# Performance work log

Measured on AMD Instinct MI355X. Metric: run time of the kernel, lower is better.

The kernel has to match this reference:

```python
import jax, jax.numpy as jnp
import numpy as np

IMG = 256          # RasterizationSettings.image_size
CHUNK = 64         # faces per scan step (bounds peak memory)
B_N, V_N, F_N = 1, 5023, 9976   # FLAME head mesh: 5023 verts / 9976 faces
BIG = 1e10
EPS = 1e-8
AMB, DIF, SPC = 0.5, 0.3, 0.2   # PointLights default ambient/diffuse/specular
SHININESS = 64.0                # Materials default shininess
LIGHT = (0.0, 0.0, 3.0)         # PointLights(location=[[0,0,3]])


def setup_inputs() -> dict:
    key = jax.random.key(0)
    kv, kf = jax.random.split(key)
    vertices = 0.15 * jax.random.normal(kv, (B_N, V_N, 3), jnp.float32)
    R = jnp.tile(jnp.eye(3, dtype=jnp.float32)[None], (B_N, 1, 1))
    T = jnp.tile(jnp.array([0.0, 0.0, 1.2], jnp.float32)[None], (B_N, 1))
    tm = jnp.zeros((B_N, 4, 4), jnp.float32)
    tm = tm.at[:, :3, :3].set(R).at[:, :3, 3].set(T).at[:, 3, 3].set(1.0)
    focal_length = jnp.full((B_N, 2), 1.5 * IMG, jnp.float32)  # screen-space focal
    faces = jax.random.randint(kf, (F_N, 3), 0, V_N, dtype=jnp.int32)
    return {"vertices": vertices, "transform_matrix": tm,
            "focal_length": focal_length, "faces": faces}


def _normalize(x):
    return x / (jnp.linalg.norm(x, axis=-1, keepdims=True) + EPS)


def _render(vertices, transform_matrix, focal_length, faces):
    B, V, _ = vertices.shape
    H = W = IMG
    HW = H * W
    R = transform_matrix[:, :3, :3]
    T = transform_matrix[:, :3, 3]

    # world -> view (PyTorch3D row-vector convention), then pinhole NDC projection
    v_view = jnp.einsum('bvi,bij->bvj', vertices, R) + T[:, None, :]
    z = v_view[..., 2]                                   # [B,V] view-space depth
    zc = jnp.maximum(z, EPS)
    fx = (2.0 * focal_length[:, 0] / W)[:, None]         # screen -> NDC focal
    fy = (2.0 * focal_length[:, 1] / H)[:, None]
    x_ndc = fx * v_view[..., 0] / zc
    y_ndc = fy * v_view[..., 1] / zc

    # pixel grid in NDC (PyTorch3D: +X left, +Y up)
    xs = 1.0 - 2.0 * (jnp.arange(W, dtype=jnp.float32) + 0.5) / W
    ys = 1.0 - 2.0 * (jnp.arange(H, dtype=jnp.float32) + 0.5) / H
    px = jnp.broadcast_to(xs[None, :], (H, W)).reshape(HW)
    py = jnp.broadcast_to(ys[:, None], (H, W)).reshape(HW)

    # pad faces to a multiple of CHUNK; gather per-face vertex coords
    F = faces.shape[0]
    nC = -(-F // CHUNK)
    Fp = nC * CHUNK
    fpad = jnp.concatenate([faces, jnp.zeros((Fp - F, 3), faces.dtype)], axis=0)
    fvalid = (jnp.arange(Fp) < F).reshape(nC, CHUNK)
    tri_x = x_ndc[:, fpad].reshape(B, nC, CHUNK, 3).transpose(1, 0, 2, 3)
    tri_y = y_ndc[:, fpad].reshape(B, nC, CHUNK, 3).transpose(1, 0, 2, 3)
    tri_z = z[:, fpad].reshape(B, nC, CHUNK, 3).transpose(1, 0, 2, 3)
    fidx = jnp.arange(Fp, dtype=jnp.int32).reshape(nC, CHUNK)

    # hard z-buffer rasterization (faces_per_pixel=1, blur_radius=0) via scan
    def step(carry, inp):
        zbuf, bestf, bb0, bb1 = carry
        tx, ty, tz, valid, fid = inp                    # tx/ty/tz: [B,CHUNK,3]
        x0, x1, x2 = (tx[..., i][:, None, :] for i in range(3))   # [B,1,C]
        y0, y1, y2 = (ty[..., i][:, None, :] for i in range(3))
        area = (x1 - x0) * (y2 - y0) - (x2 - x0) * (y1 - y0)
        P, Q = px[None, :, None], py[None, :, None]     # [1,HW,1]
        w0 = (x1 - P) * (y2 - Q) - (x2 - P) * (y1 - Q)  # [B,HW,C] edge fns
        w1 = (x2 - P) * (y0 - Q) - (x0 - P) * (y2 - Q)
        w2 = area - w0 - w1
        denom = jnp.where(jnp.abs(area) > EPS, area, 1.0)
        b0, b1, b2 = w0 / denom, w1 / denom, w2 / denom
        z0, z1, z2 = (jnp.maximum(tz[..., i], EPS)[:, None, :] for i in range(3))
        zok = (tz > EPS).all(-1)[:, None, :]
        inside = ((b0 >= 0) & (b1 >= 0) & (b2 >= 0)
                  & (jnp.abs(area) > EPS) & zok & valid[None, None, :])
        t0, t1 = b0 / z0, b1 / z1
        invz = t0 + t1 + b2 / z2
        zpix = 1.0 / jnp.maximum(invz, EPS)             # perspective-correct depth
        depth = jnp.where(inside, zpix, BIG)
        j = jnp.argmin(depth, axis=2)                   # nearest face in chunk [B,HW]
        d = jnp.take_along_axis(depth, j[..., None], 2)[..., 0]
        p0 = jnp.take_along_axis(t0 * zpix, j[..., None], 2)[..., 0]
        p1 = jnp.take_along_axis(t1 * zpix, j[..., None], 2)[..., 0]
        fh = fid[j]
        keep = d < zbuf
        return (jnp.where(keep, d, zbuf), jnp.where(keep, fh, bestf),
                jnp.where(keep, p0, bb0), jnp.where(keep, p1, bb1)), None

    init = (jnp.full((B, HW), BIG, jnp.float32), jnp.zeros((B, HW), jnp.int32),
            jnp.zeros((B, HW), jnp.float32), jnp.zeros((B, HW), jnp.float32))
    (zbuf, bestf, b0, b1), _ = jax.lax.scan(step, init, (tri_x, tri_y, tri_z, fvalid, fidx))
    hit = zbuf < (0.5 * BIG)
    bary = jnp.stack([b0, b1, 1.0 - b0 - b1], axis=-1)  # [B,HW,3] persp-correct

    # vertex normals (area-weighted face-normal scatter)
    fverts = vertices[:, faces]                         # [B,F,3,3]
    fnorm = jnp.cross(fverts[:, :, 1] - fverts[:, :, 0],
                      fverts[:, :, 2] - fverts[:, :, 0])
    vn = jnp.zeros_like(vertices)
    for i in range(3):
        vn = vn.at[:, faces[:, i]].add(fnorm)
    vn = _normalize(vn)

    # per-pixel interpolation + SoftPhongShader math (white vertex texture)
    pf = fpad[bestf]                                    # [B,HW,3] vertex ids
    gather = jax.vmap(lambda tbl, idx: tbl[idx])        # ([V,3],[HW,3])->[HW,3,3]
    pv = gather(vertices, pf)
    pn = gather(vn, pf)
    Pw = jnp.einsum('bpk,bpkc->bpc', bary, pv)          # world position
    Nw = _normalize(jnp.einsum('bpk,bpkc->bpc', bary, pn))
    cam = -jnp.einsum('bj,bkj->bk', T, R)               # camera center (R orthonormal)
    Ld = _normalize(jnp.array(LIGHT, jnp.float32)[None, None] - Pw)
    Vd = _normalize(cam[:, None] - Pw)
    ndl = jnp.maximum(jnp.sum(Nw * Ld, -1), 0.0)
    refl = -Ld + 2.0 * jnp.sum(Nw * Ld, -1, keepdims=True) * Nw
    spec = jnp.maximum(jnp.sum(refl * Vd, -1), 0.0) ** SHININESS
    shade = AMB + DIF * ndl + SPC * spec                # equal across RGB channels
    rgb = jnp.broadcast_to(shade[..., None], (B, HW, 3))
    alpha = hit.astype(jnp.float32)
    rgb = jnp.where(hit[..., None], rgb, 1.0)           # white background
    rgb = jnp.where(alpha[..., None] < 0.5, 0.0, rgb) * 255.0  # images[alpha<0.5]=0; *255
    images = rgb.reshape(B, H, W, 3).transpose(0, 3, 1, 2)
    return images, alpha.reshape(B, 1, H, W)


def reference(vertices, transform_matrix, focal_length, faces):
    return _render(vertices, transform_matrix, focal_length, faces)
```

## Files before the change

### kernel.cpp

```cpp
#include <hip/hip_runtime.h>
#include <math.h>

#define IMGSZ 256
#define HW (IMGSZ * IMGSZ)
#define EPSF 1e-8f
#define BIGF 1e10f
#define SLICE_LEN 1024
#define MARG 1e-4f
#define CAP 8192
#define SEGLEN 128
#define RBLOCKS 2048
#define SENTINEL 0x501502F9FFFFFFFFull

__global__ void k_transform(const float* __restrict__ verts,
                            const float* __restrict__ tm,
                            const float* __restrict__ focal,
                            float* __restrict__ xn, float* __restrict__ yn,
                            float* __restrict__ zv, float* __restrict__ vnacc,
                            unsigned long long* __restrict__ zb,
                            int* __restrict__ cnt, int V) {
#pragma clang fp contract(off)
    int i = blockIdx.x * blockDim.x + threadIdx.x;
    int nth = gridDim.x * blockDim.x;
    for (int j = i; j < HW; j += nth) zb[j] = SENTINEL;
    if (i < 256) cnt[i] = 0;
    if (i >= V) return;
    float vx = verts[i * 3 + 0], vy = verts[i * 3 + 1], vz = verts[i * 3 + 2];
    float xv = ((vx * tm[0] + vy * tm[4]) + vz * tm[8]) + tm[3];
    float yv = ((vx * tm[1] + vy * tm[5]) + vz * tm[9]) + tm[7];
    float zw = ((vx * tm[2] + vy * tm[6]) + vz * tm[10]) + tm[11];
    float zc = fmaxf(zw, EPSF);
    float fx = 2.0f * focal[0] / (float)IMGSZ;
    float fy = 2.0f * focal[1] / (float)IMGSZ;
    xn[i] = fx * xv / zc;
    yn[i] = fy * yv / zc;
    zv[i] = zw;
    vnacc[i * 3 + 0] = 0.0f;
    vnacc[i * 3 + 1] = 0.0f;
    vnacc[i * 3 + 2] = 0.0f;
}

__global__ void k_facesetup(const int* __restrict__ faces,
                            const float* __restrict__ verts,
                            const float* __restrict__ xn,
                            const float* __restrict__ yn,
                            const float* __restrict__ zv,
                            float4* __restrict__ fd,
                            float* __restrict__ vnacc, int F) {
#pragma clang fp contract(off)
    int f = blockIdx.x * blockDim.x + threadIdx.x;
    if (f >= F) return;
    int i0 = faces[f * 3 + 0], i1 = faces[f * 3 + 1], i2 = faces[f * 3 + 2];
    float x0 = xn[i0], x1 = xn[i1], x2 = xn[i2];
    float y0 = yn[i0], y1 = yn[i1], y2 = yn[i2];
    float z0 = zv[i0], z1 = zv[i1], z2 = zv[i2];
    float area = (x1 - x0) * (y2 - y0) - (x2 - x0) * (y1 - y0);
    bool zok = (z0 > EPSF) && (z1 > EPSF) && (z2 > EPSF);
    float areaStore = zok ? area : 0.0f;
    float z0c = fmaxf(z0, EPSF), z1c = fmaxf(z1, EPSF), z2c = fmaxf(z2, EPSF);
    float zminb = fminf(fminf(z0c, z1c), z2c) * (1.0f - 1e-5f);
    fd[f * 3 + 0] = make_float4(x0, y0, x1, y1);
    fd[f * 3 + 1] = make_float4(x2, y2, areaStore, __int_as_float(f));
    fd[f * 3 + 2] = make_float4(z0c, z1c, z2c, zminb);
    float a0 = verts[i0 * 3 + 0], a1 = verts[i0 * 3 + 1], a2 = verts[i0 * 3 + 2];
    float b0 = verts[i1 * 3 + 0], b1 = verts[i1 * 3 + 1], b2 = verts[i1 * 3 + 2];
    float c0 = verts[i2 * 3 + 0], c1 = verts[i2 * 3 + 1], c2 = verts[i2 * 3 + 2];
    float e1x = b0 - a0, e1y = b1 - a1, e1z = b2 - a2;
    float e2x = c0 - a0, e2y = c1 - a1, e2z = c2 - a2;
    float nx = e1y * e2z - e1z * e2y;
    float ny = e1z * e2x - e1x * e2z;
    float nz = e1x * e2y - e1y * e2x;
    atomicAdd(&vnacc[i0 * 3 + 0], nx);
    atomicAdd(&vnacc[i0 * 3 + 1], ny);
    atomicAdd(&vnacc[i0 * 3 + 2], nz);
    atomicAdd(&vnacc[i1 * 3 + 0], nx);
    atomicAdd(&vnacc[i1 * 3 + 1], ny);
    atomicAdd(&vnacc[i1 * 3 + 2], nz);
    atomicAdd(&vnacc[i2 * 3 + 0], nx);
    atomicAdd(&vnacc[i2 * 3 + 1], ny);
    atomicAdd(&vnacc[i2 * 3 + 2], nz);
}

__device__ __forceinline__ void tile_bounds(int tileX, int tileY,
                                            float& txmin, float& txmax,
                                            float& tymin, float& tymax) {
#pragma clang fp contract(off)
    txmax = 1.0f - 2.0f * ((float)(tileX * 16) + 0.5f) / (float)IMGSZ;
    txmin = 1.0f - 2.0f * ((float)(tileX * 16 + 15) + 0.5f) / (float)IMGSZ;
    tymax = 1.0f - 2.0f * ((float)(tileY * 16) + 0.5f) / (float)IMGSZ;
    tymin = 1.0f - 2.0f * ((float)(tileY * 16 + 15) + 0.5f) / (float)IMGSZ;
}

__device__ __forceinline__ int zbucket(float zminb) {
    float v = (zminb - 0.4f) * 40.0f;
    int b = (int)v;
    if (v < 0.0f) b = 0;
    if (b > 63) b = 63;
    return b;
}
__device__ __forceinline__ float bucketlo(float zminb) {
    int b = zbucket(zminb);
    return (b == 0) ? 0.0f : (0.4f + 0.025f * (float)b - 1e-4f);
}

__device__ __forceinline__ bool rect_cull(float x0, float y0, float x1, float y1,
                                          float x2, float y2, float area,
                                          float rxmin, float rxmax,
                                          float rymin, float rymax) {
#pragma clang fp contract(off)
    const float M = 1e-4f;
    float mnx = fminf(fminf(x0, x1), x2);
    float mxx = fmaxf(fmaxf(x0, x1), x2);
    float mny = fminf(fminf(y0, y1), y2);
    float mxy = fmaxf(fmaxf(y0, y1), y2);
    bool pass = (mnx <= rxmax + M) && (mxx >= rxmin - M) &&
                (mny <= rymax + M) && (mxy >= rymin - M);
    if (!pass) return false;
    float a0 = y1 - y2, bb0 = x2 - x1, k0 = x1 * y2 - x2 * y1;
    float a1 = y2 - y0, bb1 = x0 - x2, k1 = x2 * y0 - x0 * y2;
    float a2 = y0 - y1, bb2 = x1 - x0, k2 = x0 * y1 - x1 * y0;
    if (area > 0.0f) {
        float w0m = k0 + fmaxf(a0 * rxmin, a0 * rxmax) + fmaxf(bb0 * rymin, bb0 * rymax);
        float w1m = k1 + fmaxf(a1 * rxmin, a1 * rxmax) + fmaxf(bb1 * rymin, bb1 * rymax);
        float w2m = k2 + fmaxf(a2 * rxmin, a2 * rxmax) + fmaxf(bb2 * rymin, bb2 * rymax);
        return (w0m >= -MARG) && (w1m >= -MARG) && (w2m >= -MARG);
    } else {
        float w0m = k0 + fminf(a0 * rxmin, a0 * rxmax) + fminf(bb0 * rymin, bb0 * rymax);
        float w1m = k1 + fminf(a1 * rxmin, a1 * rxmax) + fminf(bb1 * rymin, bb1 * rymax);
        float w2m = k2 + fminf(a2 * rxmin, a2 * rxmax) + fminf(bb2 * rymin, bb2 * rymax);
        return (w0m <= MARG) && (w1m <= MARG) && (w2m <= MARG);
    }
}

__launch_bounds__(256)
__global__ void k_bincull(const float4* __restrict__ fd, int F,
                          int* __restrict__ cnt, int* __restrict__ bins,
                          unsigned long long* __restrict__ zb) {
#pragma clang fp contract(off)
    __shared__ int scnt[4];
    __shared__ int sbase;
    int t = threadIdx.x;
    int lane = t & 63, wid = t >> 6;
    int tile = blockIdx.x >> 2;
    int q = blockIdx.x & 3;
    int tileX = tile & 15, tileY = tile >> 4;
    float txmin, txmax, tymin, tymax;
    tile_bounds(tileX, tileY, txmin, txmax, tymin, tymax);
    int Fq = (F + 3) >> 2;
    int fbeg = q * Fq;
    int fend = min(F, fbeg + Fq);
    int binbase = tile * CAP;

    for (int base = fbeg; base < fend; base += 256) {
        int f = base + t;
        bool pass = false;
        float x0, y0, x1, y1, x2, y2, area;
        float4 Bv;
        if (f < fend) {
            float4 A = fd[f * 3 + 0];
            Bv = fd[f * 3 + 1];
            area = Bv.z;
            if (fabsf(area) > EPSF) {
                x0 = A.x; y0 = A.y; x1 = A.z; y1 = A.w; x2 = Bv.x; y2 = Bv.y;
                pass = rect_cull(x0, y0, x1, y1, x2, y2, area,
                                 txmin, txmax, tymin, tymax);
            }
        }
        unsigned long long m = __ballot(pass);
        if (lane == 0) scnt[wid] = __popcll(m);
        __syncthreads();
        int off = 0;
#pragma unroll
        for (int w = 0; w < 4; ++w)
            if (w < wid) off += scnt[w];
        int total = scnt[0] + scnt[1] + scnt[2] + scnt[3];
        if (t == 0) sbase = (total > 0) ? atomicAdd(&cnt[tile], total) : 0;
        __syncthreads();
        int sb = sbase;
        if (pass) {
            int rank = __popcll(m & ((1ull << lane) - 1ull));
            int s = sb + off + rank;
            if (s < CAP) {
                bins[binbase + s] = f;
            } else {
                float4 c = fd[f * 3 + 2];
                for (int p = 0; p < 256; ++p) {
                    int colp = tileX * 16 + (p & 15), rowp = tileY * 16 + (p >> 4);
                    float P = 1.0f - 2.0f * ((float)colp + 0.5f) / (float)IMGSZ;
                    float Q = 1.0f - 2.0f * ((float)rowp + 0.5f) / (float)IMGSZ;
                    float e0x = x0 - P, e0y = y0 - Q;
                    float e1x = x1 - P, e1y = y1 - Q;
                    float e2x = x2 - P, e2y = y2 - Q;
                    float w0 = e1x * e2y - e2x * e1y;
                    float w1 = e2x * e0y - e0x * e2y;
                    float w2 = (area - w0) - w1;
                    bool inside = (area > 0.0f) ? (w0 >= 0.0f && w1 >= 0.0f && w2 >= 0.0f)
                                                : (w0 <= 0.0f && w1 <= 0.0f && w2 <= 0.0f);
                    if (inside) {
                        float b0v = w0 / area, b1v = w1 / area, b2v = w2 / area;
                        float t0 = b0v / c.x, t1 = b1v / c.y, t2v = b2v / c.z;
                        float invz = (t0 + t1) + t2v;
                        float zpix = 1.0f / fmaxf(invz, EPSF);
                        unsigned long long pk =
                            ((unsigned long long)(unsigned int)__float_as_int(zpix) << 32) |
                            (unsigned int)__float_as_int(Bv.w);
                        atomicMin(&zb[rowp * IMGSZ + colp], pk);
                    }
                }
            }
        }
        __syncthreads();
    }
}

__launch_bounds__(256)
__global__ void k_binsort(const float* __restrict__ fdf,
                          const int* __restrict__ cnt,
                          int* __restrict__ bins,
                          unsigned short* __restrict__ workl,
                          int* __restrict__ worktotal) {
    __shared__ int sfid[CAP];
    __shared__ unsigned char sbkt[CAP];
    __shared__ int hist[64], hbase[64];
    __shared__ int sn[256], snseg[256], sord[256], spre[256];
    int t = threadIdx.x;
    if (blockIdx.x == 256) {
        int n = cnt[t];
        if (n > CAP) n = CAP;
        int ns = (n > 0) ? (n + SEGLEN - 1) / SEGLEN : 0;
        sn[t] = n;
        snseg[t] = ns;
        __syncthreads();
        int r = 0;
        for (int k = 0; k < 256; ++k) {
            int nk = sn[k];
            r += (nk > n) || (nk == n && k < t);
        }
        sord[r] = t;
        __syncthreads();
        if (t == 0) {
            int run = 0;
            for (int k = 0; k < 256; ++k) { spre[k] = run; run += snseg[sord[k]]; }
            *worktotal = run;
        }
        __syncthreads();
        int tile = sord[t];
        int base = spre[t];
        int ns2 = snseg[tile];
        for (int seg = 0; seg < ns2; ++seg)
            workl[base + seg] = (unsigned short)((tile << 6) | seg);
        return;
    }
    int tile = blockIdx.x;
    int n = cnt[tile];
    if (n > CAP) n = CAP;
    if (n == 0) return;
    int nseg = (n + SEGLEN - 1) / SEGLEN;
    if (t < 64) hist[t] = 0;
    __syncthreads();
    for (int i = t; i < n; i += 256) {
        int f = bins[tile * CAP + i];
        sfid[i] = f;
        float zminb = fdf[f * 12 + 11];
        int b = zbucket(zminb);
        sbkt[i] = (unsigned char)b;
        atomicAdd(&hist[b], 1);
    }
    __syncthreads();
    if (t == 0) {
        int run = 0;
        for (int k = 0; k < 64; ++k) { hbase[k] = run; run += hist[k]; }
    }
    __syncthreads();
    if (t < 64) hist[t] = 0;
    __syncthreads();
    for (int i = t; i < n; i += 256) {
        int b = sbkt[i];
        int pos = hbase[b] + atomicAdd(&hist[b], 1);
        int tpos = (pos % nseg) * SEGLEN + pos / nseg;
        bins[tile * CAP + tpos] = sfid[i];
    }
}

__launch_bounds__(256)
__global__ void k_rastseg(const float4* __restrict__ fd,
                          const int* __restrict__ cnt,
                          const int* __restrict__ bins,
                          const unsigned short* __restrict__ workl,
                          const int* __restrict__ worktotal,
                          unsigned long long* __restrict__ zb) {
#pragma clang fp contract(off)
    __shared__ float4 sA[64], sB[64], sC[64];
    __shared__ int sdone[4];
    int total = *worktotal;
    int wave = threadIdx.x >> 6;
    int lane = threadIdx.x & 63;
    int t = threadIdx.x;
    for (int wi = blockIdx.x; wi < total; wi += gridDim.x) {
        int w = workl[wi];
        int tile = w >> 6, seg = w & 63;
        int n = cnt[tile];
        if (n > CAP) n = CAP;
        int nseg = (n + SEGLEN - 1) / SEGLEN;
        int nb = (n - 1 - seg) / nseg + 1;
        int binbase = tile * CAP + seg * SEGLEN;

        int tileX = tile & 15, tileY = tile >> 4;
        int col0 = tileX * 16 + ((wave & 1) << 3);
        int row0 = tileY * 16 + ((wave >> 1) << 3);
        int col = col0 + (lane & 7);
        int row = row0 + (lane >> 3);
        int pix = row * IMGSZ + col;
        float P = 1.0f - 2.0f * ((float)col + 0.5f) / (float)IMGSZ;
        float Q = 1.0f - 2.0f * ((float)row + 0.5f) / (float)IMGSZ;
        float sxmax = 1.0f - 2.0f * ((float)col0 + 0.5f) / (float)IMGSZ;
        float sxmin = 1.0f - 2.0f * ((float)(col0 + 7) + 0.5f) / (float)IMGSZ;
        float symax = 1.0f - 2.0f * ((float)row0 + 0.5f) / (float)IMGSZ;
        float symin = 1.0f - 2.0f * ((float)(row0 + 7) + 0.5f) / (float)IMGSZ;

        unsigned long long seed = zb[pix];
        unsigned long long bestpk = seed;
        float bestz = __uint_as_float((unsigned int)(seed >> 32));
        bool done = false;
        if (lane == 0) sdone[wave] = 0;

        for (int k0 = 0; k0 < nb; k0 += 64) {
            int cnum = min(64, nb - k0);
            __syncthreads();
            if (sdone[0] + sdone[1] + sdone[2] + sdone[3] == 4) break;
            if (t < 192) {
                int part = t >> 6, fi = t & 63;
                if (fi < cnum) {
                    int f = bins[binbase + k0 + fi];
                    float4 v = fd[f * 3 + part];
                    if (part == 0) sA[fi] = v;
                    else if (part == 1) sB[fi] = v;
                    else sC[fi] = v;
                }
            }
            __syncthreads();
            if (!done) {
                bool pass8 = false;
                if (lane < cnum) {
                    float4 ra = sA[lane], rb = sB[lane];
                    float area = rb.z;
                    if (fabsf(area) > EPSF)
                        pass8 = rect_cull(ra.x, ra.y, ra.z, ra.w, rb.x, rb.y,
                                          area, sxmin, sxmax, symin, symax);
                }
                unsigned long long mm = __ballot(pass8);
                int it = 0;
                while (mm) {
                    int s = __ffsll(mm) - 1;
                    mm &= mm - 1;
                    float4 cc = sC[s];
                    if ((it++ & 7) == 0) {
                        if (__all(bucketlo(cc.w) > bestz)) {
                            done = true;
                            if (lane == 0) sdone[wave] = 1;
                            break;
                        }
                    }
                    float4 a = sA[s], b = sB[s];
                    float area = b.z;
                    float e0x = a.x - P, e0y = a.y - Q;
                    float e1x = a.z - P, e1y = a.w - Q;
                    float e2x = b.x - P, e2y = b.y - Q;
                    float w0 = e1x * e2y - e2x * e1y;
                    float w1 = e2x * e0y - e0x * e2y;
                    float w2 = (area - w0) - w1;
                    bool inside = (area > 0.0f) ? (w0 >= 0.0f && w1 >= 0.0f && w2 >= 0.0f)
                                                : (w0 <= 0.0f && w1 <= 0.0f && w2 <= 0.0f);
                    bool want = inside && !(cc.w > bestz);
                    if (want) {
                        float b0v = w0 / area, b1v = w1 / area, b2v = w2 / area;
                        float t0 = b0v / cc.x, t1 = b1v / cc.y, t2v = b2v / cc.z;
                        float invz = (t0 + t1) + t2v;
                        float zpix = 1.0f / fmaxf(invz, EPSF);
                        unsigned long long pk =
                            ((unsigned long long)(unsigned int)__float_as_int(zpix) << 32) |
                            (unsigned int)__float_as_int(b.w);
                        if (pk < bestpk) {
                            bestpk = pk;
                            bestz = zpix;
                        }
                    }
                }
            }
        }
        if (bestpk < seed) atomicMin(&zb[pix], bestpk);
        __syncthreads();
    }
}

__launch_bounds__(256)
__global__ void k_raster_mono(const float4* __restrict__ fd, int F,
                              unsigned long long* __restrict__ zb) {
#pragma clang fp contract(off)
    __shared__ float4 sfd[256 * 3];
    __shared__ int scnt[4];
    int t = threadIdx.x;
    int lane = t & 63, wid = t >> 6;
    int tile = blockIdx.x & 255;
    int slice = blockIdx.x >> 8;
    int tileX = tile & 15, tileY = tile >> 4;
    int col = tileX * 16 + (t & 15);
    int row = tileY * 16 + (t >> 4);
    int pix = row * IMGSZ + col;
    float P = 1.0f - 2.0f * ((float)col + 0.5f) / (float)IMGSZ;
    float Q = 1.0f - 2.0f * ((float)row + 0.5f) / (float)IMGSZ;
    float txmin, txmax, tymin, tymax;
    tile_bounds(tileX, tileY, txmin, txmax, tymin, tymax);
    int fbeg = slice * SLICE_LEN;
    int fend = fbeg + SLICE_LEN;
    if (fend > F) fend = F;
    unsigned long long bestpk = SENTINEL;
    float bestz = BIGF;
    for (int base = fbeg; base < fend; base += 256) {
        unsigned long long ext = zb[pix];
        if (ext < bestpk) {
            bestpk = ext;
            bestz = __uint_as_float((unsigned int)(ext >> 32));
        }
        int f = base + t;
        bool pass = false;
        float4 A, B, C;
        if (f < fend) {
            A = fd[f * 3 + 0];
            B = fd[f * 3 + 1];
            C = fd[f * 3 + 2];
            float area = B.z;
            if (fabsf(area) > EPSF)
                pass = rect_cull(A.x, A.y, A.z, A.w, B.x, B.y, area,
                                 txmin, txmax, tymin, tymax);
        }
        unsigned long long m = __ballot(pass);
        if (lane == 0) scnt[wid] = __popcll(m);
        __syncthreads();
        int off = 0;
#pragma unroll
        for (int w = 0; w < 4; ++w)
            if (w < wid) off += scnt[w];
        int total = scnt[0] + scnt[1] + scnt[2] + scnt[3];
        if (pass) {
            int rank = __popcll(m & ((1ull << lane) - 1ull));
            int s = off + rank;
            sfd[s * 3 + 0] = A;
            sfd[s * 3 + 1] = B;
            sfd[s * 3 + 2] = C;
        }
        __syncthreads();
        for (int s = 0; s < total; ++s) {
            float4 a = sfd[s * 3 + 0], b = sfd[s * 3 + 1], c = sfd[s * 3 + 2];
            float e0x = a.x - P, e0y = a.y - Q;
            float e1x = a.z - P, e1y = a.w - Q;
            float e2x = b.x - P, e2y = b.y - Q;
            float w0 = e1x * e2y - e2x * e1y;
            float w1 = e2x * e0y - e0x * e2y;
            float area = b.z;
            float w2 = (area - w0) - w1;
            bool inside = (area > 0.0f) ? (w0 >= 0.0f && w1 >= 0.0f && w2 >= 0.0f)
                                        : (w0 <= 0.0f && w1 <= 0.0f && w2 <= 0.0f);
            bool want = inside && !(c.w > bestz);
            if (want) {
                float b0v = w0 / area, b1v = w1 / area, b2v = w2 / area;
                float t0 = b0v / c.x, t1 = b1v / c.y, t2v = b2v / c.z;
                float invz = (t0 + t1) + t2v;
                float zpix = 1.0f / fmaxf(invz, EPSF);
                unsigned long long pk =
                    ((unsigned long long)(unsigned int)__float_as_int(zpix) << 32) |
                    (unsigned int)__float_as_int(b.w);
                if (pk < bestpk) {
                    bestpk = pk;
                    bestz = zpix;
                }
            }
        }
        if (bestpk < ext) atomicMin(&zb[pix], bestpk);
        __syncthreads();
    }
}

__launch_bounds__(256)
__global__ void k_shade(const unsigned long long* __restrict__ zb,
                        const float4* __restrict__ fd,
                        const int* __restrict__ faces,
                        const float* __restrict__ verts,
                        const float* __restrict__ vn,
                        const float* __restrict__ tm,
                        float* __restrict__ out) {
#pragma clang fp contract(off)
    int pix = blockIdx.x * 256 + threadIdx.x;
    unsigned long long pk = zb[pix];
    float depth = __uint_as_float((unsigned int)(pk >> 32));
    float val = 0.0f, alpha = 0.0f;
    if (depth < 0.5f * BIGF) {
        int bestf = (int)(unsigned int)(pk & 0xFFFFFFFFull);
        int col = pix & (IMGSZ - 1), row = pix >> 8;
        float P = 1.0f - 2.0f * ((float)col + 0.5f) / (float)IMGSZ;
        float Q = 1.0f - 2.0f * ((float)row + 0.5f) / (float)IMGSZ;
        float4 a = fd[bestf * 3 + 0], b = fd[bestf * 3 + 1], c = fd[bestf * 3 + 2];
        float e0x = a.x - P, e0y = a.y - Q;
        float e1x = a.z - P, e1y = a.w - Q;
        float e2x = b.x - P, e2y = b.y - Q;
        float w0 = e1x * e2y - e2x * e1y;
        float w1 = e2x * e0y - e0x * e2y;
        float area = b.z;
        float t0 = (w0 / area) / c.x, t1 = (w1 / area) / c.y;
        float t2v = (((area - w0) - w1) / area) / c.z;
        float invz = (t0 + t1) + t2v;
        float zpix = 1.0f / fmaxf(invz, EPSF);
        float bp0 = t0 * zpix, bp1 = t1 * zpix;

        int i0 = faces[bestf * 3 + 0], i1 = faces[bestf * 3 + 1], i2 = faces[bestf * 3 + 2];
        float b0v = bp0, b1v = bp1, b2v = (1.0f - bp0) - bp1;
        float Pwx = (b0v * verts[i0 * 3 + 0] + b1v * verts[i1 * 3 + 0]) + b2v * verts[i2 * 3 + 0];
        float Pwy = (b0v * verts[i0 * 3 + 1] + b1v * verts[i1 * 3 + 1]) + b2v * verts[i2 * 3 + 1];
        float Pwz = (b0v * verts[i0 * 3 + 2] + b1v * verts[i1 * 3 + 2]) + b2v * verts[i2 * 3 + 2];
        float v0x = vn[i0 * 3 + 0], v0y = vn[i0 * 3 + 1], v0z = vn[i0 * 3 + 2];
        float n0 = sqrtf((v0x * v0x + v0y * v0y) + v0z * v0z) + EPSF;
        v0x /= n0; v0y /= n0; v0z /= n0;
        float v1x = vn[i1 * 3 + 0], v1y = vn[i1 * 3 + 1], v1z = vn[i1 * 3 + 2];
        float n1 = sqrtf((v1x * v1x + v1y * v1y) + v1z * v1z) + EPSF;
        v1x /= n1; v1y /= n1; v1z /= n1;
        float v2x = vn[i2 * 3 + 0], v2y = vn[i2 * 3 + 1], v2z = vn[i2 * 3 + 2];
        float n2 = sqrtf((v2x * v2x + v2y * v2y) + v2z * v2z) + EPSF;
        v2x /= n2; v2y /= n2; v2z /= n2;
        float Nx = (b0v * v0x + b1v * v1x) + b2v * v2x;
        float Ny = (b0v * v0y + b1v * v1y) + b2v * v2y;
        float Nz = (b0v * v0z + b1v * v1z) + b2v * v2z;
        float nn = sqrtf((Nx * Nx + Ny * Ny) + Nz * Nz) + EPSF;
        Nx /= nn; Ny /= nn; Nz /= nn;
        float T0 = tm[3], T1 = tm[7], T2 = tm[11];
        float camx = -((T0 * tm[0] + T1 * tm[1]) + T2 * tm[2]);
        float camy = -((T0 * tm[4] + T1 * tm[5]) + T2 * tm[6]);
        float camz = -((T0 * tm[8] + T1 * tm[9]) + T2 * tm[10]);
        float Ldx = 0.0f - Pwx, Ldy = 0.0f - Pwy, Ldz = 3.0f - Pwz;
        float ln = sqrtf((Ldx * Ldx + Ldy * Ldy) + Ldz * Ldz) + EPSF;
        Ldx /= ln; Ldy /= ln; Ldz /= ln;
        float Vx = camx - Pwx, Vy = camy - Pwy, Vz = camz - Pwz;
        float vv = sqrtf((Vx * Vx + Vy * Vy) + Vz * Vz) + EPSF;
        Vx /= vv; Vy /= vv; Vz /= vv;
        float dt = (Nx * Ldx + Ny * Ldy) + Nz * Ldz;
        float ndl = fmaxf(dt, 0.0f);
        float twodt = 2.0f * dt;
        float rx = -Ldx + twodt * Nx;
        float ry = -Ldy + twodt * Ny;
        float rz = -Ldz + twodt * Nz;
        float sdot = (rx * Vx + ry * Vy) + rz * Vz;
        float sb = fmaxf(sdot, 0.0f);
        float s2 = sb * sb, s4 = s2 * s2, s8 = s4 * s4, s16 = s8 * s8, s32 = s16 * s16;
        float spec = s32 * s32;
        float shade = (0.5f + 0.3f * ndl) + 0.2f * spec;
        val = shade * 255.0f;
        alpha = 1.0f;
    }
    out[0 * HW + pix] = val;
    out[1 * HW + pix] = val;
    out[2 * HW + pix] = val;
    out[3 * HW + pix] = alpha;
}

extern "C" void kernel_launch(void* const* d_in, const int* in_sizes, int n_in,
                              void* d_out, int out_size, void* d_ws, size_t ws_size,
                              hipStream_t stream) {
    const float* verts = (const float*)d_in[0];
    const float* tm = (const float*)d_in[1];
    const float* focal = (const float*)d_in[2];
    const int* faces = (const int*)d_in[3];
    int V = in_sizes[0] / 3;
    int F = in_sizes[3] / 3;

    char* base = (char*)d_ws;
    unsigned long long* zb = (unsigned long long*)base;
    int* cnt = (int*)(base + (size_t)HW * 8);
    float* xn = (float*)(base + (size_t)HW * 8 + 4096);
    float* yn = xn + V;
    float* zv = xn + 2 * (size_t)V;
    float* vn = xn + 3 * (size_t)V;
    size_t fdByte = ((size_t)HW * 8 + 4096 + 6 * (size_t)V * 4 + 15) & ~(size_t)15;
    float4* fd = (float4*)(base + fdByte);
    size_t binByte = fdByte + (size_t)F * 48;
    int* bins = (int*)(base + binByte);
    size_t workByte = binByte + (size_t)256 * CAP * 4;
    unsigned short* workl = (unsigned short*)(base + workByte);
    int* worktotal = (int*)(base + workByte + 16384 * 2);
    size_t needBinned = workByte + 16384 * 2 + 64;
    float* out = (float*)d_out;

    int vb = (V + 255) / 256;
    int fb = (F + 255) / 256;
    k_transform<<<vb, 256, 0, stream>>>(verts, tm, focal, xn, yn, zv, vn, zb, cnt, V);
    k_facesetup<<<fb, 256, 0, stream>>>(faces, verts, xn, yn, zv, fd, vn, F);
    if (ws_size >= needBinned) {
        k_bincull<<<256 * 4, 256, 0, stream>>>(fd, F, cnt, bins, zb);
        k_binsort<<<257, 256, 0, stream>>>((const float*)fd, cnt, bins, workl, worktotal);
        k_rastseg<<<RBLOCKS, 256, 0, stream>>>(fd, cnt, bins, workl, worktotal, zb);
    } else {
        int nslice = (F + SLICE_LEN - 1) / SLICE_LEN;
        k_raster_mono<<<256 * nslice, 256, 0, stream>>>(fd, F, zb);
    }
    k_shade<<<HW / 256, 256, 0, stream>>>(zb, fd, faces, verts, vn, tm, out);
}
```

Baseline: 92.38 us.

## Pack per-tile conservative depth bound into bin entries for sorting and culling

The bin cull now computes, for each face/tile pair, a conservative lower bound on depth over the tile from the interpolated inverse-depth plane. It quantizes that bound and packs it with the face id into a 32-bit bin entry. The sort uses the top bits as its bucket, so it no longer gathers face depth data, and the raster loop uses the per-tile bound for wave-uniform early skipping and termination. The C record is loaded only for covered pixels. This tightens depth culling and cuts memory traffic, at the cost of extra setup math in the cull and a limit of 14 bits (16384) on face ids.

```diff
diff --git a/kernel.cpp b/kernel.cpp
--- a/kernel.cpp
+++ b/kernel.cpp
@@ -10,6 +10,7 @@
 #define CAP 8192
 #define SEGLEN 128
 #define RBLOCKS 2048
+#define QSTEP (2.0f / 262144.0f)
 #define SENTINEL 0x501502F9FFFFFFFFull
 
 __global__ void k_transform(const float* __restrict__ verts,
@@ -91,18 +92,6 @@
     tymin = 1.0f - 2.0f * ((float)(tileY * 16 + 15) + 0.5f) / (float)IMGSZ;
 }
 
-__device__ __forceinline__ int zbucket(float zminb) {
-    float v = (zminb - 0.4f) * 40.0f;
-    int b = (int)v;
-    if (v < 0.0f) b = 0;
-    if (b > 63) b = 63;
-    return b;
-}
-__device__ __forceinline__ float bucketlo(float zminb) {
-    int b = zbucket(zminb);
-    return (b == 0) ? 0.0f : (0.4f + 0.025f * (float)b - 1e-4f);
-}
-
 __device__ __forceinline__ bool rect_cull(float x0, float y0, float x1, float y1,
                                           float x2, float y2, float area,
                                           float rxmin, float rxmax,
@@ -134,7 +123,7 @@
 
 __launch_bounds__(256)
 __global__ void k_bincull(const float4* __restrict__ fd, int F,
-                          int* __restrict__ cnt, int* __restrict__ bins,
+                          int* __restrict__ cnt, unsigned* __restrict__ bins,
                           unsigned long long* __restrict__ zb) {
 #pragma clang fp contract(off)
     __shared__ int scnt[4];
@@ -154,6 +143,7 @@
     for (int base = fbeg; base < fend; base += 256) {
         int f = base + t;
         bool pass = false;
+        unsigned entry = 0;
         float x0, y0, x1, y1, x2, y2, area;
         float4 Bv;
         if (f < fend) {
@@ -164,6 +154,31 @@
                 x0 = A.x; y0 = A.y; x1 = A.z; y1 = A.w; x2 = Bv.x; y2 = Bv.y;
                 pass = rect_cull(x0, y0, x1, y1, x2, y2, area,
                                  txmin, txmax, tymin, tymax);
+                if (pass) {
+                    float4 Cv = fd[f * 3 + 2];
+                    float r0 = 1.0f / (area * Cv.x);
+                    float r1 = 1.0f / (area * Cv.y);
+                    float r2 = 1.0f / (area * Cv.z);
+                    float a0 = y1 - y2, bb0 = x2 - x1, k0 = x1 * y2 - x2 * y1;
+                    float a1 = y2 - y0, bb1 = x0 - x2, k1 = x2 * y0 - x0 * y2;
+                    float a2 = y0 - y1, bb2 = x1 - x0, k2 = x0 * y1 - x1 * y0;
+                    float K = (k0 * r0 + k1 * r1) + k2 * r2;
+                    float GX = (a0 * r0 + a1 * r1) + a2 * r2;
+                    float GY = (bb0 * r0 + bb1 * r1) + bb2 * r2;
+                    float gx = fmaxf(GX * txmin, GX * txmax);
+                    float gy = fmaxf(GY * tymin, GY * tymax);
+                    float invmax = K + gx + gy;
+                    float mag = (fabsf(k0 * r0) + fabsf(k1 * r1) + fabsf(k2 * r2))
+                              + fmaxf(fabsf(GX * txmin), fabsf(GX * txmax))
+                              + fmaxf(fabsf(GY * tymin), fabsf(GY * tymax));
+                    invmax = invmax + 1e-5f * mag;
+                    float zlo = (1.0f / fmaxf(invmax, EPSF)) * (1.0f - 1e-5f);
+                    float qf = zlo * (1.0f / QSTEP);
+                    int qz = (int)qf;
+                    if (qf < 0.0f) qz = 0;
+                    if (qz > 262143) qz = 262143;
+                    entry = ((unsigned)qz << 14) | (unsigned)f;
+                }
             }
         }
         unsigned long long m = __ballot(pass);
@@ -181,7 +196,7 @@
             int rank = __popcll(m & ((1ull << lane) - 1ull));
             int s = sb + off + rank;
             if (s < CAP) {
-                bins[binbase + s] = f;
+                bins[binbase + s] = entry;
             } else {
                 float4 c = fd[f * 3 + 2];
                 for (int p = 0; p < 256; ++p) {
@@ -214,13 +229,11 @@
 }
 
 __launch_bounds__(256)
-__global__ void k_binsort(const float* __restrict__ fdf,
-                          const int* __restrict__ cnt,
-                          int* __restrict__ bins,
+__global__ void k_binsort(const int* __restrict__ cnt,
+                          unsigned* __restrict__ bins,
                           unsigned short* __restrict__ workl,
                           int* __restrict__ worktotal) {
-    __shared__ int sfid[CAP];
-    __shared__ unsigned char sbkt[CAP];
+    __shared__ unsigned sent[CAP];
     __shared__ int hist[64], hbase[64];
     __shared__ int sn[256], snseg[256], sord[256], spre[256];
     int t = threadIdx.x;
@@ -259,12 +272,9 @@
     if (t < 64) hist[t] = 0;
     __syncthreads();
     for (int i = t; i < n; i += 256) {
-        int f = bins[tile * CAP + i];
-        sfid[i] = f;
-        float zminb = fdf[f * 12 + 11];
-        int b = zbucket(zminb);
-        sbkt[i] = (unsigned char)b;
-        atomicAdd(&hist[b], 1);
+        unsigned e = bins[tile * CAP + i];
+        sent[i] = e;
+        atomicAdd(&hist[e >> 26], 1);
     }
     __syncthreads();
     if (t == 0) {
@@ -275,22 +285,24 @@
     if (t < 64) hist[t] = 0;
     __syncthreads();
     for (int i = t; i < n; i += 256) {
-        int b = sbkt[i];
+        unsigned e = sent[i];
+        int b = e >> 26;
         int pos = hbase[b] + atomicAdd(&hist[b], 1);
         int tpos = (pos % nseg) * SEGLEN + pos / nseg;
-        bins[tile * CAP + tpos] = sfid[i];
+        bins[tile * CAP + tpos] = e;
     }
 }
 
 __launch_bounds__(256)
 __global__ void k_rastseg(const float4* __restrict__ fd,
                           const int* __restrict__ cnt,
-                          const int* __restrict__ bins,
+                          const unsigned* __restrict__ bins,
                           const unsigned short* __restrict__ workl,
                           const int* __restrict__ worktotal,
                           unsigned long long* __restrict__ zb) {
 #pragma clang fp contract(off)
     __shared__ float4 sA[64], sB[64], sC[64];
+    __shared__ unsigned sE[64];
     __shared__ int sdone[4];
     int total = *worktotal;
     int wave = threadIdx.x >> 6;
@@ -331,11 +343,11 @@
             if (t < 192) {
                 int part = t >> 6, fi = t & 63;
                 if (fi < cnum) {
-                    int f = bins[binbase + k0 + fi];
-                    float4 v = fd[f * 3 + part];
-                    if (part == 0) sA[fi] = v;
-                    else if (part == 1) sB[fi] = v;
-                    else sC[fi] = v;
+                    unsigned e = bins[binbase + k0 + fi];
+                    int fid = e & 0x3FFF;
+                    if (part == 0) { sE[fi] = e; sA[fi] = fd[fid * 3 + 0]; }
+                    else if (part == 1) sB[fi] = fd[fid * 3 + 1];
+                    else sC[fi] = fd[fid * 3 + 2];
                 }
             }
             __syncthreads();
@@ -353,13 +365,18 @@
                 while (mm) {
                     int s = __ffsll(mm) - 1;
                     mm &= mm - 1;
-                    float4 cc = sC[s];
+                    unsigned e = sE[s];
+                    float zlo = (float)(e >> 14) * QSTEP;
                     if ((it++ & 7) == 0) {
-                        if (__all(bucketlo(cc.w) > bestz)) {
+                        float blo = (float)(e >> 26) * (4096.0f * QSTEP);
+                        if (__all(blo > bestz)) {
                             done = true;
                             if (lane == 0) sdone[wave] = 1;
                             break;
                         }
+                    }
+                    if (zlo > bestz) {
+                        if (__all(zlo > bestz)) continue;
                     }
                     float4 a = sA[s], b = sB[s];
                     float area = b.z;
@@ -371,8 +388,9 @@
                     float w2 = (area - w0) - w1;
                     bool inside = (area > 0.0f) ? (w0 >= 0.0f && w1 >= 0.0f && w2 >= 0.0f)
                                                 : (w0 <= 0.0f && w1 <= 0.0f && w2 <= 0.0f);
-                    bool want = inside && !(cc.w > bestz);
+                    bool want = inside && !(zlo > bestz);
                     if (want) {
+                        float4 cc = sC[s];
                         float b0v = w0 / area, b1v = w1 / area, b2v = w2 / area;
                         float t0 = b0v / cc.x, t1 = b1v / cc.y, t2v = b2v / cc.z;
                         float invz = (t0 + t1) + t2v;
@@ -581,7 +599,7 @@
     size_t fdByte = ((size_t)HW * 8 + 4096 + 6 * (size_t)V * 4 + 15) & ~(size_t)15;
     float4* fd = (float4*)(base + fdByte);
     size_t binByte = fdByte + (size_t)F * 48;
-    int* bins = (int*)(base + binByte);
+    unsigned* bins = (unsigned*)(base + binByte);
     size_t workByte = binByte + (size_t)256 * CAP * 4;
     unsigned short* workl = (unsigned short*)(base + workByte);
     int* worktotal = (int*)(base + workByte + 16384 * 2);
@@ -594,7 +612,7 @@
     k_facesetup<<<fb, 256, 0, stream>>>(faces, verts, xn, yn, zv, fd, vn, F);
     if (ws_size >= needBinned) {
         k_bincull<<<256 * 4, 256, 0, stream>>>(fd, F, cnt, bins, zb);
-        k_binsort<<<257, 256, 0, stream>>>((const float*)fd, cnt, bins, workl, worktotal);
+        k_binsort<<<257, 256, 0, stream>>>(cnt, bins, workl, worktotal);
         k_rastseg<<<RBLOCKS, 256, 0, stream>>>(fd, cnt, bins, workl, worktotal, zb);
     } else {
         int nslice = (F + SLICE_LEN - 1) / SLICE_LEN;
```

Result: faster. 81.40 us (-11.9%).
